# Kernel tuning notes

Hardware: AMD Instinct MI355X
Metric: run time of the kernel (lower is better)

The kernel has to match this reference:

```python
import jax, jax.numpy as jnp
import numpy as np

NUM_HEADS = 32
NUM_KV_HEADS = 8
HEAD_DIM = 128
ROPE_THETA = 10000.0


def _rope(q):
    # q: [B, H, S, D]; positions 0..S-1
    S, D = q.shape[2], q.shape[3]
    inv_freq = 1.0 / (ROPE_THETA ** (jnp.arange(0, D, 2, dtype=jnp.float32) / D))
    ang = jnp.arange(S, dtype=jnp.float32)[:, None] * inv_freq[None, :]  # [S, D/2]
    emb = jnp.concatenate([ang, ang], axis=-1)                            # [S, D]
    cos, sin = jnp.cos(emb), jnp.sin(emb)
    q1, q2 = q[..., : D // 2], q[..., D // 2:]
    rot = jnp.concatenate([-q2, q1], axis=-1)
    return q * cos + rot * sin


def setup_inputs() -> dict:
    key = jax.random.key(0)
    k1, k2, k3, k4, k5 = jax.random.split(key, 5)
    B, S, H = 1, 512, 4096
    num_blocks, block_size = 1024, 16
    blocks_per_seq = 512
    return {
        "hidden_states": jax.random.normal(k1, (B, S, H), jnp.float32),
        "Wq": jax.random.normal(k2, (H, H), jnp.float32) * 0.02,
        "Wo": jax.random.normal(k3, (H, H), jnp.float32) * 0.02,
        "kv_cache": jax.random.normal(k4, (num_blocks, 2, NUM_KV_HEADS, block_size, HEAD_DIM), jnp.float32),
        "block_table": jax.random.randint(k5, (blocks_per_seq,), 0, num_blocks, jnp.int32),
    }


def reference(hidden_states, Wq, Wo, kv_cache, block_table):
    B, S, H = hidden_states.shape
    # q projection + head split: [B, nH, S, D]
    q = (hidden_states @ Wq).reshape(B, S, NUM_HEADS, HEAD_DIM).transpose(0, 2, 1, 3)
    q = _rope(q)
    # paged KV gather: [nb, 2, kvH, bs, D] -> [1, kvH, T, D]
    blocks = kv_cache[block_table]
    nb, _, kvH, bs, D = blocks.shape
    K = blocks[:, 0].transpose(1, 0, 2, 3).reshape(kvH, nb * bs, D)[None]
    V = blocks[:, 1].transpose(1, 0, 2, 3).reshape(kvH, nb * bs, D)[None]
    # GQA: repeat_interleave kv heads
    factor = NUM_HEADS // NUM_KV_HEADS
    K = jnp.repeat(K, factor, axis=1)
    V = jnp.repeat(V, factor, axis=1)
    scores = jnp.einsum("bhsd,bhtd->bhst", q, K) / jnp.sqrt(jnp.float32(HEAD_DIM))
    attn = jax.nn.softmax(scores, axis=-1)
    ctx = jnp.einsum("bhst,bhtd->bhsd", attn, V)
    ctx = ctx.transpose(0, 2, 1, 3).reshape(B, S, H)
    return ctx @ Wo
```

## Files before the change

kernel.cpp:

```cpp
#include <hip/hip_runtime.h>

typedef short bf16x8 __attribute__((ext_vector_type(8)));
typedef float f32x4 __attribute__((ext_vector_type(4)));

#define SEQ 512
#define HID 4096
#define TKV 8192
#define NS 2
#define TPS (TKV / NS)
#define KVB 64
#define NT (TPS / KVB)
#define SCALE 0.08838834764831845f

__device__ __forceinline__ ushort f2b(float f) {
  union { float f; unsigned u; } v; v.f = f;
  unsigned u = v.u;
  unsigned r = (u + 0x7FFFu + ((u >> 16) & 1u)) >> 16;
  return (ushort)r;
}

#if __has_builtin(__builtin_amdgcn_global_load_lds)
typedef __attribute__((address_space(3))) unsigned int as3_uint;
typedef const __attribute__((address_space(1))) unsigned int as1_uint;
__device__ __forceinline__ void gll16(const void* g, void* l) {
  __builtin_amdgcn_global_load_lds((as1_uint*)g, (as3_uint*)l, 16, 0, 0);
}
#else
__device__ __forceinline__ void gll16(const void* g, void* l) {
  uint4 t = *(const uint4*)g;
  *(uint4*)((char*)l + (threadIdx.x & 63) * 16) = t;
}
#endif

__global__ __launch_bounds__(256) void cvt_hidden(const float* __restrict__ in, ushort* __restrict__ out) {
  int i = (blockIdx.x * 256 + threadIdx.x) * 4;
  float4 v = *(const float4*)(in + i);
  ushort4 o; o.x = f2b(v.x); o.y = f2b(v.y); o.z = f2b(v.z); o.w = f2b(v.w);
  *(ushort4*)(out + i) = o;
}

__global__ __launch_bounds__(256) void transpose_cvt(const float* __restrict__ W, ushort* __restrict__ WT) {
  __shared__ float tile[32][33];
  int bx = blockIdx.x, by = blockIdx.y;
  int x = threadIdx.x & 31, y0 = threadIdx.x >> 5;
#pragma unroll
  for (int yy = 0; yy < 32; yy += 8)
    tile[y0 + yy][x] = W[(by * 32 + y0 + yy) * HID + bx * 32 + x];
  __syncthreads();
#pragma unroll
  for (int yy = 0; yy < 32; yy += 8)
    WT[(bx * 32 + y0 + yy) * HID + by * 32 + x] = f2b(tile[x][y0 + yy]);
}

__global__ __launch_bounds__(256) void gather_k(const float* __restrict__ cache, const int* __restrict__ btab,
                                                ushort* __restrict__ Kb) {
  int i = blockIdx.x * 256 + threadIdx.x;
  int d4  = i & 31;
  int pos = (i >> 5) & 15;
  int kvh = (i >> 9) & 7;
  int blk = i >> 12;
  int b = btab[blk];
  const float4 v = *(const float4*)(cache + (((long)(b * 2) * 8 + kvh) * 16 + pos) * 128 + d4 * 4);
  ushort4 o; o.x = f2b(v.x); o.y = f2b(v.y); o.z = f2b(v.z); o.w = f2b(v.w);
  *(ushort4*)(Kb + ((long)kvh * TKV + blk * 16 + pos) * 128 + d4 * 4) = o;
}

__global__ __launch_bounds__(256) void gather_vt(const float* __restrict__ cache, const int* __restrict__ btab,
                                                 ushort* __restrict__ Vt) {
  __shared__ __align__(16) float tile[16][132];
  int bid = blockIdx.x;
  int kvh = bid & 7, blk = bid >> 3;
  int b = btab[blk];
  const float* src = cache + (((long)(b * 2 + 1) * 8 + kvh) * 16) * 128;
  int tid = threadIdx.x;
#pragma unroll
  for (int p = 0; p < 2; p++) {
    int idx = tid + p * 256;
    int pos = idx >> 5, c4 = idx & 31;
    float4 v = *(const float4*)(src + pos * 128 + c4 * 4);
    *(float4*)&tile[pos][c4 * 4] = v;
  }
  __syncthreads();
  int d = tid >> 1, half = tid & 1;
  bf16x8 pk;
#pragma unroll
  for (int j = 0; j < 8; j++) pk[j] = (short)f2b(tile[half * 8 + j][d]);
  *(bf16x8*)(Vt + ((long)kvh * 128 + d) * TKV + blk * 16 + half * 8) = pk;
}

__global__ __launch_bounds__(256) void rope_table(float* __restrict__ ct, float* __restrict__ st) {
  int i = blockIdx.x * 256 + threadIdx.x;
  int s = i >> 6, j = i & 63;
  double invf = exp(-((double)(2 * j) / 128.0) * log(10000.0));
  double ang = (double)s * invf;
  ct[i] = (float)cos(ang);
  st[i] = (float)sin(ang);
}

__global__ __launch_bounds__(256) void rope_apply(const float* __restrict__ Qt, const float* __restrict__ ct,
                                                  const float* __restrict__ st, ushort* __restrict__ Qb) {
  int i = blockIdx.x * 256 + threadIdx.x;
  int s = i >> 12;
  int hd = i & 4095;
  int h = hd >> 7, d = hd & 127;
  int j = d & 63;
  float c = ct[s * 64 + j], sn = st[s * 64 + j];
  float q = Qt[i];
  float qp = Qt[(d < 64) ? (i + 64) : (i - 64)];
  float rot = (d < 64) ? -qp : qp;
  Qb[((long)h * SEQ + s) * 128 + d] = f2b(q * c + rot * sn);
}

__global__ __launch_bounds__(256, 1) void gemm2(const ushort* __restrict__ A, const ushort* __restrict__ BT,
                                                float* __restrict__ C, int M, int N, int K) {
  __shared__ __align__(16) ushort As[2][64 * 64];
  __shared__ __align__(16) ushort Bs[2][128 * 64];
  const int bm = blockIdx.x, bn = blockIdx.y;
  const int tid = threadIdx.x, lane = tid & 63, w = tid >> 6;
  const int wm = w >> 1, wn = w & 1;
  const int l15 = lane & 15, lg = lane >> 4;
  const int xr = l15 & 7;
  const int sr = lane >> 3, sc = lane & 7;
  f32x4 acc[2][4] = {};

#define GSTAGE(B, KT) do {                                                            \
    _Pragma("unroll") for (int i_ = 0; i_ < 2; i_++) {                                \
      int r0 = (w * 2 + i_) * 8; int r = r0 + sr;                                     \
      gll16(A + (long)(bm * 64 + r) * K + (KT) + ((sc ^ (r & 7)) * 8), &As[B][r0 * 64]); } \
    _Pragma("unroll") for (int i_ = 0; i_ < 4; i_++) {                                \
      int r0 = (w * 4 + i_) * 8; int r = r0 + sr;                                     \
      gll16(BT + (long)(bn * 128 + r) * K + (KT) + ((sc ^ (r & 7)) * 8), &Bs[B][r0 * 64]); } \
  } while (0)

  GSTAGE(0, 0);
  __syncthreads();
  int buf = 0;
  for (int kt = 0; kt < K; kt += 64) {
    if (kt + 64 < K) GSTAGE(buf ^ 1, kt + 64);
#pragma unroll
    for (int kk = 0; kk < 2; kk++) {
      bf16x8 af[2], bfr[4];
#pragma unroll
      for (int m = 0; m < 2; m++) {
        int row = wm * 32 + m * 16 + l15;
        af[m] = *(const bf16x8*)(&As[buf][row * 64 + (((kk * 4 + lg) ^ xr) * 8)]);
      }
#pragma unroll
      for (int n = 0; n < 4; n++) {
        int row = wn * 64 + n * 16 + l15;
        bfr[n] = *(const bf16x8*)(&Bs[buf][row * 64 + (((kk * 4 + lg) ^ xr) * 8)]);
      }
#pragma unroll
      for (int m = 0; m < 2; m++)
#pragma unroll
        for (int n = 0; n < 4; n++)
          acc[m][n] = __builtin_amdgcn_mfma_f32_16x16x32_bf16(af[m], bfr[n], acc[m][n], 0, 0, 0);
    }
    __syncthreads();
    buf ^= 1;
  }
#pragma unroll
  for (int m = 0; m < 2; m++)
#pragma unroll
    for (int n = 0; n < 4; n++)
#pragma unroll
      for (int r = 0; r < 4; r++) {
        int row = bm * 64 + wm * 32 + m * 16 + lg * 4 + r;
        int col = bn * 128 + wn * 64 + n * 16 + l15;
        C[(long)row * N + col] = acc[m][n][r];
      }
#undef GSTAGE
}

__global__ __launch_bounds__(512, 1) void attn2(const ushort* __restrict__ Q, const ushort* __restrict__ Kc,
                                                const ushort* __restrict__ Vt, float* __restrict__ Op,
                                                float* __restrict__ ml) {
  __shared__ __align__(16) ushort Ks[2][64 * 128];
  __shared__ __align__(16) ushort Vs[2][128 * 64];
  __shared__ __align__(16) ushort Ps[8][16 * 72];
  const int bid = blockIdx.x;
  const int kvh = bid & 7;
  const int y = bid >> 3;
  const int ns = y >> 4;
  const int qb = (y >> 1) & 7;
  const int hpi = y & 1;
  const int tid = threadIdx.x, lane = tid & 63, w = tid >> 6;
  const int head = kvh * 4 + hpi * 2 + (w >> 2);
  const int wrow = (w & 3) * 16;
  const int l15 = lane & 15, lg = lane >> 4;
  const int xq = l15 & 7;
  const int kr = lane >> 4, kc = lane & 15;
  const int vr = lane >> 3, vc = lane & 7;
  const ushort* Kg = Kc + ((long)kvh * TKV + ns * TPS) * 128;
  const ushort* Vg = Vt + (long)kvh * 128 * TKV + ns * TPS;

  bf16x8 qf[4];
  {
    const ushort* qrow = Q + ((long)head * SEQ + qb * 64 + wrow + l15) * 128 + lg * 8;
#pragma unroll
    for (int kk = 0; kk < 4; kk++) qf[kk] = *(const bf16x8*)(qrow + kk * 32);
  }
  f32x4 o[8] = {};
  float mrow[4] = {-3e38f, -3e38f, -3e38f, -3e38f};
  float srow[4] = {0.f, 0.f, 0.f, 0.f};

#define STAGE(B, T0) do {                                                         \
    _Pragma("unroll") for (int i_ = 0; i_ < 2; i_++) {                            \
      int r0 = (w * 2 + i_) * 4; int r = r0 + kr;                                 \
      gll16(Kg + (long)((T0) + r) * 128 + ((kc ^ (r & 7)) * 8), &Ks[B][r0 * 128]); } \
    _Pragma("unroll") for (int i_ = 0; i_ < 2; i_++) {                            \
      int r0 = (w * 2 + i_) * 8; int r = r0 + vr;                                 \
      gll16(Vg + (long)r * TKV + (T0) + ((vc ^ (r & 7)) * 8), &Vs[B][r0 * 64]); } \
  } while (0)

  STAGE(0, 0);
  __syncthreads();
  int buf = 0;
  for (int t = 0; t < NT; t++) {
    if (t + 1 < NT) STAGE(buf ^ 1, (t + 1) * KVB);
    f32x4 s[4] = {};
#pragma unroll
    for (int kk = 0; kk < 4; kk++)
#pragma unroll
      for (int n = 0; n < 4; n++) {
        int row = n * 16 + l15;
        bf16x8 kf = *(const bf16x8*)(&Ks[buf][row * 128 + (((kk * 4 + lg) ^ xq) * 8)]);
        s[n] = __builtin_amdgcn_mfma_f32_16x16x32_bf16(qf[kk], kf, s[n], 0, 0, 0);
      }
    float pp[4][4];
#pragma unroll
    for (int r = 0; r < 4; r++) {
      float a = fmaxf(fmaxf(s[0][r], s[1][r]), fmaxf(s[2][r], s[3][r])) * SCALE;
#pragma unroll
      for (int m_ = 1; m_ < 16; m_ <<= 1) a = fmaxf(a, __shfl_xor(a, m_, 64));
      float mn = fmaxf(mrow[r], a);
      float al = __expf(mrow[r] - mn);
      mrow[r] = mn;
      float ls = 0.f;
#pragma unroll
      for (int n = 0; n < 4; n++) { float p = __expf(s[n][r] * SCALE - mn); pp[n][r] = p; ls += p; }
      srow[r] = srow[r] * al + ls;
#pragma unroll
      for (int n8 = 0; n8 < 8; n8++) o[n8][r] *= al;
    }
#pragma unroll
    for (int n = 0; n < 4; n++)
#pragma unroll
      for (int r = 0; r < 4; r++)
        Ps[w][(lg * 4 + r) * 72 + n * 16 + l15] = f2b(pp[n][r]);
#pragma unroll
    for (int kk = 0; kk < 2; kk++) {
      bf16x8 pf = *(const bf16x8*)(&Ps[w][l15 * 72 + kk * 32 + lg * 8]);
#pragma unroll
      for (int n8 = 0; n8 < 8; n8++) {
        int row = n8 * 16 + l15;
        bf16x8 vf = *(const bf16x8*)(&Vs[buf][row * 64 + (((kk * 4 + lg) ^ xq) * 8)]);
        o[n8] = __builtin_amdgcn_mfma_f32_16x16x32_bf16(pf, vf, o[n8], 0, 0, 0);
      }
    }
    __syncthreads();
    buf ^= 1;
  }
#undef STAGE
#pragma unroll
  for (int r = 0; r < 4; r++) {
    float rs = srow[r];
#pragma unroll
    for (int m_ = 1; m_ < 16; m_ <<= 1) rs += __shfl_xor(rs, m_, 64);
    int qg = qb * 64 + wrow + lg * 4 + r;
    float* ob = Op + ((long)(ns * 32 + head) * SEQ + qg) * 128;
#pragma unroll
    for (int n8 = 0; n8 < 8; n8++) ob[n8 * 16 + l15] = o[n8][r];
    if (l15 == 0) {
      float* mp = ml + ((long)(ns * 32 + head) * SEQ + qg) * 2;
      mp[0] = mrow[r];
      mp[1] = rs;
    }
  }
}

__global__ __launch_bounds__(256) void merge2(const float* __restrict__ Op, const float* __restrict__ ml,
                                              ushort* __restrict__ Cx) {
  int i = blockIdx.x * 256 + threadIdx.x;
  int d4 = i & 31, h = (i >> 5) & 31, q = i >> 10;
  long b0 = (long)h * SEQ + q;
  long b1 = (long)(32 + h) * SEQ + q;
  float m0 = ml[b0 * 2], l0 = ml[b0 * 2 + 1];
  float m1 = ml[b1 * 2], l1 = ml[b1 * 2 + 1];
  float ma = fmaxf(m0, m1);
  float w0 = __expf(m0 - ma), w1 = __expf(m1 - ma);
  float inv = 1.f / (l0 * w0 + l1 * w1);
  float4 o0 = *(const float4*)(Op + b0 * 128 + d4 * 4);
  float4 o1 = *(const float4*)(Op + b1 * 128 + d4 * 4);
  ushort4 r;
  r.x = f2b((o0.x * w0 + o1.x * w1) * inv);
  r.y = f2b((o0.y * w0 + o1.y * w1) * inv);
  r.z = f2b((o0.z * w0 + o1.z * w1) * inv);
  r.w = f2b((o0.w * w0 + o1.w * w1) * inv);
  *(ushort4*)(Cx + (long)q * HID + h * 128 + d4 * 4) = r;
}

extern "C" void kernel_launch(void* const* d_in, const int* in_sizes, int n_in,
                              void* d_out, int out_size, void* d_ws, size_t ws_size,
                              hipStream_t stream) {
  const float* hidden = (const float*)d_in[0];
  const float* Wq = (const float*)d_in[1];
  const float* Wo = (const float*)d_in[2];
  const float* cache = (const float*)d_in[3];
  const int* btab = (const int*)d_in[4];
  float* out = (float*)d_out;
  char* ws = (char*)d_ws;

  ushort* WqT = (ushort*)(ws);
  float*  Op  = (float*)(ws);
  float*  ml  = (float*)(ws + 16777216);
  ushort* WoT = (ushort*)(ws + 33554432);
  ushort* Kb  = (ushort*)(ws + 67108864);
  ushort* Vt  = (ushort*)(ws + 83886080);
  ushort* Xb  = (ushort*)(ws + 100663296);
  float*  Qt  = (float*)(ws + 104857600);
  ushort* Qb  = (ushort*)(ws + 113246208);
  ushort* Cx  = (ushort*)(ws + 117440512);
  float*  ct  = (float*)(ws + 121634816);
  float*  st  = (float*)(ws + 121765888);

  cvt_hidden<<<dim3(2048), dim3(256), 0, stream>>>(hidden, Xb);
  transpose_cvt<<<dim3(128, 128), dim3(256), 0, stream>>>(Wq, WqT);
  transpose_cvt<<<dim3(128, 128), dim3(256), 0, stream>>>(Wo, WoT);
  gather_k<<<dim3(8192), dim3(256), 0, stream>>>(cache, btab, Kb);
  gather_vt<<<dim3(4096), dim3(256), 0, stream>>>(cache, btab, Vt);
  rope_table<<<dim3(128), dim3(256), 0, stream>>>(ct, st);
  gemm2<<<dim3(8, 32), dim3(256), 0, stream>>>(Xb, WqT, Qt, 512, 4096, 4096);
  rope_apply<<<dim3(8192), dim3(256), 0, stream>>>(Qt, ct, st, Qb);
  attn2<<<dim3(256), dim3(512), 0, stream>>>(Qb, Kb, Vt, Op, ml);
  merge2<<<dim3(2048), dim3(256), 0, stream>>>(Op, ml, Cx);
  gemm2<<<dim3(8, 32), dim3(256), 0, stream>>>(Cx, WoT, out, 512, 4096, 4096);
}
```

Baseline: 576.9 us.

## Merge weight transposes, shrink GEMM/attention blocks, add lazy softmax rescaling

Merges the two weight transpose-convert launches into one kernel that uses 64x64 tiles and vectorized 16-byte stores. The GEMM output tile shrinks to 64x64 and attention blocks drop to 256 threads with one head each, both with launch bounds allowing two blocks per CU, to get more blocks and occupancy. The softmax scale is folded into Q during RoPE, and the running-max rescale now runs only when some row's max grows by more than 8. That skips shuffles and rescaling on most tiles, at the cost of exponents up to e^8 before normalization. An explicit LDS waitcnt is added before the P reads.

```diff
diff --git a/kernel.cpp b/kernel.cpp
--- a/kernel.cpp
+++ b/kernel.cpp
@@ -39,17 +39,30 @@
   *(ushort4*)(out + i) = o;
 }
 
-__global__ __launch_bounds__(256) void transpose_cvt(const float* __restrict__ W, ushort* __restrict__ WT) {
-  __shared__ float tile[32][33];
+__global__ __launch_bounds__(256) void transpose_cvt2(const float* __restrict__ Wq, ushort* __restrict__ WqT,
+                                                      const float* __restrict__ Wo, ushort* __restrict__ WoT) {
+  __shared__ __align__(16) float tile[64][68];
+  const float* W = blockIdx.z ? Wo : Wq;
+  ushort* WT = blockIdx.z ? WoT : WqT;
   int bx = blockIdx.x, by = blockIdx.y;
-  int x = threadIdx.x & 31, y0 = threadIdx.x >> 5;
-#pragma unroll
-  for (int yy = 0; yy < 32; yy += 8)
-    tile[y0 + yy][x] = W[(by * 32 + y0 + yy) * HID + bx * 32 + x];
+  int tid = threadIdx.x;
+#pragma unroll
+  for (int p = 0; p < 4; p++) {
+    int idx = tid + p * 256;
+    int r = idx >> 4, c4 = (idx & 15) * 4;
+    *(float4*)&tile[r][c4] = *(const float4*)(W + (long)(by * 64 + r) * HID + bx * 64 + c4);
+  }
   __syncthreads();
-#pragma unroll
-  for (int yy = 0; yy < 32; yy += 8)
-    WT[(bx * 32 + y0 + yy) * HID + by * 32 + x] = f2b(tile[x][y0 + yy]);
+  int r = tid >> 2, q = tid & 3;
+  bf16x8 a, b;
+#pragma unroll
+  for (int j = 0; j < 8; j++) {
+    a[j] = (short)f2b(tile[q * 16 + j][r]);
+    b[j] = (short)f2b(tile[q * 16 + 8 + j][r]);
+  }
+  long ob = (long)(bx * 64 + r) * HID + by * 64 + q * 16;
+  *(bf16x8*)(WT + ob) = a;
+  *(bf16x8*)(WT + ob + 8) = b;
 }
 
 __global__ __launch_bounds__(256) void gather_k(const float* __restrict__ cache, const int* __restrict__ btab,
@@ -108,28 +121,28 @@
   float q = Qt[i];
   float qp = Qt[(d < 64) ? (i + 64) : (i - 64)];
   float rot = (d < 64) ? -qp : qp;
-  Qb[((long)h * SEQ + s) * 128 + d] = f2b(q * c + rot * sn);
-}
-
-__global__ __launch_bounds__(256, 1) void gemm2(const ushort* __restrict__ A, const ushort* __restrict__ BT,
+  Qb[((long)h * SEQ + s) * 128 + d] = f2b((q * c + rot * sn) * SCALE);
+}
+
+__global__ __launch_bounds__(256, 2) void gemm3(const ushort* __restrict__ A, const ushort* __restrict__ BT,
                                                 float* __restrict__ C, int M, int N, int K) {
   __shared__ __align__(16) ushort As[2][64 * 64];
-  __shared__ __align__(16) ushort Bs[2][128 * 64];
+  __shared__ __align__(16) ushort Bs[2][64 * 64];
   const int bm = blockIdx.x, bn = blockIdx.y;
   const int tid = threadIdx.x, lane = tid & 63, w = tid >> 6;
   const int wm = w >> 1, wn = w & 1;
   const int l15 = lane & 15, lg = lane >> 4;
   const int xr = l15 & 7;
   const int sr = lane >> 3, sc = lane & 7;
-  f32x4 acc[2][4] = {};
-
-#define GSTAGE(B, KT) do {                                                            \
-    _Pragma("unroll") for (int i_ = 0; i_ < 2; i_++) {                                \
-      int r0 = (w * 2 + i_) * 8; int r = r0 + sr;                                     \
+  f32x4 acc[2][2] = {};
+
+#define GSTAGE(B, KT) do {                                                              \
+    _Pragma("unroll") for (int i_ = 0; i_ < 2; i_++) {                                  \
+      int r0 = (w * 2 + i_) * 8; int r = r0 + sr;                                       \
       gll16(A + (long)(bm * 64 + r) * K + (KT) + ((sc ^ (r & 7)) * 8), &As[B][r0 * 64]); } \
-    _Pragma("unroll") for (int i_ = 0; i_ < 4; i_++) {                                \
-      int r0 = (w * 4 + i_) * 8; int r = r0 + sr;                                     \
-      gll16(BT + (long)(bn * 128 + r) * K + (KT) + ((sc ^ (r & 7)) * 8), &Bs[B][r0 * 64]); } \
+    _Pragma("unroll") for (int i_ = 0; i_ < 2; i_++) {                                  \
+      int r0 = (w * 2 + i_) * 8; int r = r0 + sr;                                       \
+      gll16(BT + (long)(bn * 64 + r) * K + (KT) + ((sc ^ (r & 7)) * 8), &Bs[B][r0 * 64]); } \
   } while (0)
 
   GSTAGE(0, 0);
@@ -139,21 +152,21 @@
     if (kt + 64 < K) GSTAGE(buf ^ 1, kt + 64);
 #pragma unroll
     for (int kk = 0; kk < 2; kk++) {
-      bf16x8 af[2], bfr[4];
+      bf16x8 af[2], bfr[2];
 #pragma unroll
       for (int m = 0; m < 2; m++) {
         int row = wm * 32 + m * 16 + l15;
         af[m] = *(const bf16x8*)(&As[buf][row * 64 + (((kk * 4 + lg) ^ xr) * 8)]);
       }
 #pragma unroll
-      for (int n = 0; n < 4; n++) {
-        int row = wn * 64 + n * 16 + l15;
+      for (int n = 0; n < 2; n++) {
+        int row = wn * 32 + n * 16 + l15;
         bfr[n] = *(const bf16x8*)(&Bs[buf][row * 64 + (((kk * 4 + lg) ^ xr) * 8)]);
       }
 #pragma unroll
       for (int m = 0; m < 2; m++)
 #pragma unroll
-        for (int n = 0; n < 4; n++)
+        for (int n = 0; n < 2; n++)
           acc[m][n] = __builtin_amdgcn_mfma_f32_16x16x32_bf16(af[m], bfr[n], acc[m][n], 0, 0, 0);
     }
     __syncthreads();
@@ -162,31 +175,31 @@
 #pragma unroll
   for (int m = 0; m < 2; m++)
 #pragma unroll
-    for (int n = 0; n < 4; n++)
+    for (int n = 0; n < 2; n++)
 #pragma unroll
       for (int r = 0; r < 4; r++) {
         int row = bm * 64 + wm * 32 + m * 16 + lg * 4 + r;
-        int col = bn * 128 + wn * 64 + n * 16 + l15;
+        int col = bn * 64 + wn * 32 + n * 16 + l15;
         C[(long)row * N + col] = acc[m][n][r];
       }
 #undef GSTAGE
 }
 
-__global__ __launch_bounds__(512, 1) void attn2(const ushort* __restrict__ Q, const ushort* __restrict__ Kc,
+__global__ __launch_bounds__(256, 2) void attn3(const ushort* __restrict__ Q, const ushort* __restrict__ Kc,
                                                 const ushort* __restrict__ Vt, float* __restrict__ Op,
                                                 float* __restrict__ ml) {
   __shared__ __align__(16) ushort Ks[2][64 * 128];
   __shared__ __align__(16) ushort Vs[2][128 * 64];
-  __shared__ __align__(16) ushort Ps[8][16 * 72];
+  __shared__ __align__(16) ushort Ps[4][16 * 72];
   const int bid = blockIdx.x;
   const int kvh = bid & 7;
   const int y = bid >> 3;
-  const int ns = y >> 4;
-  const int qb = (y >> 1) & 7;
-  const int hpi = y & 1;
+  const int ns = y >> 5;
+  const int qb = (y >> 2) & 7;
+  const int hpi = y & 3;
+  const int head = kvh * 4 + hpi;
   const int tid = threadIdx.x, lane = tid & 63, w = tid >> 6;
-  const int head = kvh * 4 + hpi * 2 + (w >> 2);
-  const int wrow = (w & 3) * 16;
+  const int wrow = w * 16;
   const int l15 = lane & 15, lg = lane >> 4;
   const int xq = l15 & 7;
   const int kr = lane >> 4, kc = lane & 15;
@@ -205,11 +218,11 @@
   float srow[4] = {0.f, 0.f, 0.f, 0.f};
 
 #define STAGE(B, T0) do {                                                         \
-    _Pragma("unroll") for (int i_ = 0; i_ < 2; i_++) {                            \
-      int r0 = (w * 2 + i_) * 4; int r = r0 + kr;                                 \
+    _Pragma("unroll") for (int i_ = 0; i_ < 4; i_++) {                            \
+      int r0 = (w * 4 + i_) * 4; int r = r0 + kr;                                 \
       gll16(Kg + (long)((T0) + r) * 128 + ((kc ^ (r & 7)) * 8), &Ks[B][r0 * 128]); } \
-    _Pragma("unroll") for (int i_ = 0; i_ < 2; i_++) {                            \
-      int r0 = (w * 2 + i_) * 8; int r = r0 + vr;                                 \
+    _Pragma("unroll") for (int i_ = 0; i_ < 4; i_++) {                            \
+      int r0 = (w * 4 + i_) * 8; int r = r0 + vr;                                 \
       gll16(Vg + (long)r * TKV + (T0) + ((vc ^ (r & 7)) * 8), &Vs[B][r0 * 64]); } \
   } while (0)
 
@@ -227,27 +240,40 @@
         bf16x8 kf = *(const bf16x8*)(&Ks[buf][row * 128 + (((kk * 4 + lg) ^ xq) * 8)]);
         s[n] = __builtin_amdgcn_mfma_f32_16x16x32_bf16(qf[kk], kf, s[n], 0, 0, 0);
       }
+    float m4[4];
+#pragma unroll
+    for (int r = 0; r < 4; r++)
+      m4[r] = fmaxf(fmaxf(s[0][r], s[1][r]), fmaxf(s[2][r], s[3][r]));
+    float dmax = fmaxf(fmaxf(m4[0] - mrow[0], m4[1] - mrow[1]),
+                       fmaxf(m4[2] - mrow[2], m4[3] - mrow[3]));
+    if (!__all(dmax <= 8.0f)) {
+#pragma unroll
+      for (int r = 0; r < 4; r++) {
+        float a = m4[r];
+#pragma unroll
+        for (int m_ = 1; m_ < 16; m_ <<= 1) a = fmaxf(a, __shfl_xor(a, m_, 64));
+        float mn = fmaxf(mrow[r], a);
+        float al = __expf(mrow[r] - mn);
+        mrow[r] = mn;
+        srow[r] *= al;
+#pragma unroll
+        for (int n8 = 0; n8 < 8; n8++) o[n8][r] *= al;
+      }
+    }
     float pp[4][4];
 #pragma unroll
     for (int r = 0; r < 4; r++) {
-      float a = fmaxf(fmaxf(s[0][r], s[1][r]), fmaxf(s[2][r], s[3][r])) * SCALE;
-#pragma unroll
-      for (int m_ = 1; m_ < 16; m_ <<= 1) a = fmaxf(a, __shfl_xor(a, m_, 64));
-      float mn = fmaxf(mrow[r], a);
-      float al = __expf(mrow[r] - mn);
-      mrow[r] = mn;
       float ls = 0.f;
 #pragma unroll
-      for (int n = 0; n < 4; n++) { float p = __expf(s[n][r] * SCALE - mn); pp[n][r] = p; ls += p; }
-      srow[r] = srow[r] * al + ls;
-#pragma unroll
-      for (int n8 = 0; n8 < 8; n8++) o[n8][r] *= al;
+      for (int n = 0; n < 4; n++) { float p = __expf(s[n][r] - mrow[r]); pp[n][r] = p; ls += p; }
+      srow[r] += ls;
     }
 #pragma unroll
     for (int n = 0; n < 4; n++)
 #pragma unroll
       for (int r = 0; r < 4; r++)
         Ps[w][(lg * 4 + r) * 72 + n * 16 + l15] = f2b(pp[n][r]);
+    asm volatile("s_waitcnt lgkmcnt(0)" ::: "memory");
 #pragma unroll
     for (int kk = 0; kk < 2; kk++) {
       bf16x8 pf = *(const bf16x8*)(&Ps[w][l15 * 72 + kk * 32 + lg * 8]);
@@ -325,14 +351,13 @@
   float*  st  = (float*)(ws + 121765888);
 
   cvt_hidden<<<dim3(2048), dim3(256), 0, stream>>>(hidden, Xb);
-  transpose_cvt<<<dim3(128, 128), dim3(256), 0, stream>>>(Wq, WqT);
-  transpose_cvt<<<dim3(128, 128), dim3(256), 0, stream>>>(Wo, WoT);
+  transpose_cvt2<<<dim3(64, 64, 2), dim3(256), 0, stream>>>(Wq, WqT, Wo, WoT);
   gather_k<<<dim3(8192), dim3(256), 0, stream>>>(cache, btab, Kb);
   gather_vt<<<dim3(4096), dim3(256), 0, stream>>>(cache, btab, Vt);
   rope_table<<<dim3(128), dim3(256), 0, stream>>>(ct, st);
-  gemm2<<<dim3(8, 32), dim3(256), 0, stream>>>(Xb, WqT, Qt, 512, 4096, 4096);
+  gemm3<<<dim3(8, 64), dim3(256), 0, stream>>>(Xb, WqT, Qt, 512, 4096, 4096);
   rope_apply<<<dim3(8192), dim3(256), 0, stream>>>(Qt, ct, st, Qb);
-  attn2<<<dim3(256), dim3(512), 0, stream>>>(Qb, Kb, Vt, Op, ml);
+  attn3<<<dim3(512), dim3(256), 0, stream>>>(Qb, Kb, Vt, Op, ml);
   merge2<<<dim3(2048), dim3(256), 0, stream>>>(Op, ml, Cx);
-  gemm2<<<dim3(8, 32), dim3(256), 0, stream>>>(Cx, WoT, out, 512, 4096, 4096);
-}
+  gemm3<<<dim3(8, 64), dim3(256), 0, stream>>>(Cx, WoT, out, 512, 4096, 4096);
+}
```

After: 520.8 us. -9.7%, faster.
